# Optimization experiments

Hardware: AMD Instinct MI355X
Metric: run time of the kernel (lower is better)

## Reference

```python
import jax, jax.numpy as jnp
import numpy as np

N_HEADS, D_MODEL, D_HEAD = 16, 1024, 64
BATCH, SEQ = 8, 1024
INIT_RANGE = 0.02
IGNORE = -100000.0


def setup_inputs() -> dict:
    key = jax.random.key(0)
    ks = jax.random.split(key, 6)
    return {
        "normalized_resid_pre": jax.random.normal(ks[0], (BATCH, SEQ, D_MODEL), jnp.float32),
        "encoder_output": jax.random.normal(ks[1], (BATCH, SEQ, D_MODEL), jnp.float32),
        "Qs": jax.random.normal(ks[2], (N_HEADS, D_MODEL, D_HEAD), jnp.float32) * INIT_RANGE,
        "Qbs": jnp.zeros((N_HEADS, D_HEAD), jnp.float32),
        "Ks": jax.random.normal(ks[3], (N_HEADS, D_MODEL, D_HEAD), jnp.float32) * INIT_RANGE,
        "Kbs": jnp.zeros((N_HEADS, D_HEAD), jnp.float32),
        "Vs": jax.random.normal(ks[4], (N_HEADS, D_MODEL, D_HEAD), jnp.float32) * INIT_RANGE,
        "Vbs": jnp.zeros((N_HEADS, D_HEAD), jnp.float32),
        "O": jax.random.normal(ks[5], (N_HEADS, D_HEAD, D_MODEL), jnp.float32) * INIT_RANGE,
        "Ob": jnp.zeros((D_MODEL,), jnp.float32),
    }


def reference(normalized_resid_pre, encoder_output, Qs, Qbs, Ks, Kbs, Vs, Vbs, O, Ob):
    sqrt_d_head = np.sqrt(D_HEAD).astype(np.float32)
    # per-head projections: q,k from encoder_output, v from normalized_resid_pre
    q = jnp.einsum('bpd,hdk->bphk', encoder_output, Qs) + Qbs
    k = jnp.einsum('bpd,hdk->bphk', encoder_output, Ks) + Kbs
    v = jnp.einsum('bpd,hdk->bphk', normalized_resid_pre, Vs) + Vbs
    # [B,H,Q,K] scores, scaled then causally masked with -1e5 (not -inf)
    scores = jnp.einsum('bqhk,bmhk->bhqm', q, k) / sqrt_d_head
    causal = jnp.triu(jnp.ones((SEQ, SEQ), bool), k=1)
    scores = jnp.where(causal, jnp.float32(IGNORE), scores)
    attn = jax.nn.softmax(scores, axis=-1)
    z = jnp.einsum('bmhk,bhqm->bqhk', v, attn)
    return jnp.einsum('bqhk,hkd->bqd', z, O) + Ob
```

## Files before the change

kernel.cpp:

```cpp
#include <hip/hip_runtime.h>
#include <hip/hip_bf16.h>
#include <cstdint>
#include <cstddef>
#include <math.h>


typedef __attribute__((ext_vector_type(8))) short short8;
typedef __attribute__((ext_vector_type(4))) short short4v;
typedef __attribute__((ext_vector_type(4))) float f32x4;

#define MFMA16(A, B, C) __builtin_amdgcn_mfma_f32_16x16x32_bf16(A, B, C, 0, 0, 0)

__device__ inline short f2bs(float f) {
    __bf16 h = (__bf16)f;
    return __builtin_bit_cast(short, h);
}

typedef const __attribute__((address_space(1))) unsigned int* as1_u32p;
typedef __attribute__((address_space(3))) unsigned int* as3_u32p;

__device__ inline void gload_lds16(const void* g, void* lds_base) {
    __builtin_amdgcn_global_load_lds((as1_u32p)(uintptr_t)g,
                                     (as3_u32p)(uintptr_t)lds_base, 16, 0, 0);
}

#define ATTN_SC 0.18033688f
#define ATTN_THR 11.5415603f

__global__ __launch_bounds__(256) void cvt_k(const float* __restrict__ a,
                                             const float* __restrict__ b,
                                             short* __restrict__ oa,
                                             short* __restrict__ ob) {
    const int n = 8 * 1024 * 1024;
    const float* src = blockIdx.y ? b : a;
    short* dst = blockIdx.y ? ob : oa;
    for (int i = (blockIdx.x * 256 + threadIdx.x) * 8; i < n; i += gridDim.x * 256 * 8) {
        f32x4 v0 = *(const f32x4*)(src + i), v1 = *(const f32x4*)(src + i + 4);
        short8 o;
        o[0] = f2bs(v0[0]); o[1] = f2bs(v0[1]); o[2] = f2bs(v0[2]); o[3] = f2bs(v0[3]);
        o[4] = f2bs(v1[0]); o[5] = f2bs(v1[1]); o[6] = f2bs(v1[2]); o[7] = f2bs(v1[3]);
        *(short8*)(dst + i) = o;
    }
}

__global__ __launch_bounds__(256) void wtrans_k(
    const float* __restrict__ Wq, const float* __restrict__ Wk,
    const float* __restrict__ Wv, const float* __restrict__ Wo,
    short* __restrict__ TQ, short* __restrict__ TK,
    short* __restrict__ TV, short* __restrict__ TO) {
    __shared__ short tile[64][72];
    const int wsel = blockIdx.y;
    const float* in = wsel == 0 ? Wq : wsel == 1 ? Wk : wsel == 2 ? Wv : Wo;
    short* out = wsel == 0 ? TQ : wsel == 1 ? TK : wsel == 2 ? TV : TO;
    const int h = blockIdx.x >> 4, tk = blockIdx.x & 15;
    const int t = threadIdx.x;
    size_t ioff; int istr, orow0, ocol0;
    if (wsel < 3) { ioff = (size_t)h * 65536 + (size_t)tk * 64 * 64; istr = 64;   orow0 = h * 64;  ocol0 = tk * 64; }
    else          { ioff = (size_t)h * 65536 + (size_t)tk * 64;      istr = 1024; orow0 = tk * 64; ocol0 = h * 64; }
    {
        const int r = t >> 2, c0 = (t & 3) * 16;
        const float* src = in + ioff + (size_t)r * istr + c0;
#pragma unroll
        for (int j = 0; j < 4; j++) {
            f32x4 v = *(const f32x4*)(src + j * 4);
            tile[r][c0 + j * 4 + 0] = f2bs(v[0]);
            tile[r][c0 + j * 4 + 1] = f2bs(v[1]);
            tile[r][c0 + j * 4 + 2] = f2bs(v[2]);
            tile[r][c0 + j * 4 + 3] = f2bs(v[3]);
        }
    }
    __syncthreads();
    {
        const int cc = t >> 2, rb = (t & 3) * 16;
        short8 o0, o1;
#pragma unroll
        for (int j = 0; j < 8; j++) { o0[j] = tile[rb + j][cc]; o1[j] = tile[rb + 8 + j][cc]; }
        short* dst = out + (size_t)(orow0 + cc) * 1024 + ocol0 + rb;
        *(short8*)dst = o0;
        *(short8*)(dst + 8) = o1;
    }
}

template <int MODE>
__global__ __launch_bounds__(256) void gemm_bt(const short* __restrict__ A,
                                               const short* __restrict__ B,
                                               const float* __restrict__ bias,
                                               void* __restrict__ Cp,
                                               const float* __restrict__ bias2,
                                               void* __restrict__ Cp2) {
    constexpr int K = 1024;
    __shared__ short As[128 * 64];
    __shared__ short Bs[128 * 64];
    const int t = threadIdx.x, l = t & 63, w = t >> 6, lr = l & 15, lg = l >> 4;
    const int wm = (w >> 1) * 64, wn = (w & 1) * 64;
    const int m0 = blockIdx.x * 128, n0 = blockIdx.y * 128;
    const int sr = l >> 3, cb = l & 7;
    f32x4 acc[4][4] = {};

    for (int k0 = 0; k0 < K; k0 += 64) {
#pragma unroll
        for (int i = 0; i < 4; i++) {
            const int c = w * 4 + i, r = c * 8 + sr, cbs = cb ^ (r & 7);
            gload_lds16(A + (size_t)(m0 + r) * K + k0 + cbs * 8, &As[c * 512]);
        }
#pragma unroll
        for (int i = 0; i < 4; i++) {
            const int c = w * 4 + i, r = c * 8 + sr, cbs = cb ^ (r & 7);
            gload_lds16(B + (size_t)(n0 + r) * K + k0 + cbs * 8, &Bs[c * 512]);
        }
        __syncthreads();
#pragma unroll
        for (int kk = 0; kk < 2; kk++) {
            short8 af[4], bf[4];
#pragma unroll
            for (int mi = 0; mi < 4; mi++) {
                const int r = wm + mi * 16 + lr;
                af[mi] = *(const short8*)&As[r * 64 + ((kk * 4 + lg) ^ (r & 7)) * 8];
            }
#pragma unroll
            for (int nj = 0; nj < 4; nj++) {
                const int r = wn + nj * 16 + lr;
                bf[nj] = *(const short8*)&Bs[r * 64 + ((kk * 4 + lg) ^ (r & 7)) * 8];
            }
#pragma unroll
            for (int mi = 0; mi < 4; mi++)
#pragma unroll
                for (int nj = 0; nj < 4; nj++)
                    acc[mi][nj] = MFMA16(af[mi], bf[nj], acc[mi][nj]);
        }
        __syncthreads();
    }

#pragma unroll
    for (int mi = 0; mi < 4; mi++) {
#pragma unroll
        for (int nj = 0; nj < 4; nj++) {
            const int col = n0 + wn + nj * 16 + lr;
            if (MODE == 3) {
                const int h2 = col >> 6;
                short* dst = (short*)(h2 < 16 ? Cp : Cp2);
                const float bv = h2 < 16 ? bias[col & 1023] : bias2[col & 1023];
                const float sc = h2 < 16 ? ATTN_SC : 1.0f;
                const int h = h2 & 15, d = col & 63;
#pragma unroll
                for (int e = 0; e < 4; e++) {
                    const int row = m0 + wm + mi * 16 + lg * 4 + e;
                    const int bb = row >> 10, s = row & 1023;
                    dst[((size_t)(bb * 16 + h) * 1024 + s) * 64 + d] =
                        f2bs((acc[mi][nj][e] + bv) * sc);
                }
            } else if (MODE == 2) {
                const float bv = bias[col];
                const int rowb = m0 + wm + mi * 16 + lg * 4;
                const int bb = rowb >> 10, s0 = rowb & 1023;
                const int h = col >> 6, d = col & 63;
                short4v pk;
#pragma unroll
                for (int e = 0; e < 4; e++) pk[e] = f2bs(acc[mi][nj][e] + bv);
                *(short4v*)((short*)Cp + ((size_t)(bb * 16 + h) * 64 + d) * 1024 + s0) = pk;
            } else {
                const float bv = bias[col];
#pragma unroll
                for (int e = 0; e < 4; e++) {
                    const int row = m0 + wm + mi * 16 + lg * 4 + e;
                    ((float*)Cp)[(size_t)row * 1024 + col] = acc[mi][nj][e] + bv;
                }
            }
        }
    }
}

template <bool DIAG>
__device__ __forceinline__ void attn_tile(
    const short* __restrict__ Ks, const short* __restrict__ Vt,
    short (*__restrict__ Psw)[76],
    const short8* __restrict__ qf, float* __restrict__ m,
    float* __restrict__ ps, f32x4* __restrict__ acc,
    int lr, int lg, int rowloc) {
    f32x4 sf[4];
#pragma unroll
    for (int n = 0; n < 4; n++) {
        const int rk = n * 16 + lr;
        short8 kf0 = *(const short8*)&Ks[rk * 64 + ((lg) ^ (rk & 7)) * 8];
        short8 kf1 = *(const short8*)&Ks[rk * 64 + ((4 + lg) ^ (rk & 7)) * 8];
        f32x4 s = {};
        s = MFMA16(qf[0], kf0, s);
        s = MFMA16(qf[1], kf1, s);
        sf[n] = s;
    }
    if (DIAG) {
#pragma unroll
        for (int n = 0; n < 4; n++)
#pragma unroll
            for (int e = 0; e < 4; e++)
                if (n * 16 + lr > rowloc + e) sf[n][e] = -1e30f;
    }
    float pm[4];
#pragma unroll
    for (int e = 0; e < 4; e++)
        pm[e] = fmaxf(fmaxf(sf[0][e], sf[1][e]), fmaxf(sf[2][e], sf[3][e]));
    bool ok = true;
#pragma unroll
    for (int e = 0; e < 4; e++) ok = ok && (pm[e] <= m[e] + ATTN_THR);
    if (!__all(ok)) {
#pragma unroll
        for (int e = 0; e < 4; e++) {
            float tm = pm[e];
#pragma unroll
            for (int off = 1; off < 16; off <<= 1)
                tm = fmaxf(tm, __shfl_xor(tm, off));
            float nm = fmaxf(m[e], tm);
            float al = exp2f(m[e] - nm);
            m[e] = nm;
            ps[e] *= al;
#pragma unroll
            for (int n4 = 0; n4 < 4; n4++) acc[n4][e] *= al;
        }
    }
#pragma unroll
    for (int e = 0; e < 4; e++) {
#pragma unroll
        for (int n = 0; n < 4; n++) {
            float p = exp2f(sf[n][e] - m[e]);
            ps[e] += p;
            Psw[lg * 4 + e][n * 16 + lr] = f2bs(p);
        }
    }
#pragma unroll
    for (int c = 0; c < 2; c++) {
        short8 pf = *(const short8*)&Psw[lr][lg * 8 + c * 32];
#pragma unroll
        for (int n4 = 0; n4 < 4; n4++) {
            const int rv = n4 * 16 + lr;
            short8 vf = *(const short8*)&Vt[rv * 64 + ((lg + 4 * c) ^ (rv & 7)) * 8];
            acc[n4] = MFMA16(pf, vf, acc[n4]);
        }
    }
}

__global__ __launch_bounds__(256, 4) void attn_k(const short* __restrict__ Q,
                                                 const short* __restrict__ Kp,
                                                 const short* __restrict__ Vg,
                                                 short* __restrict__ Z) {
    __shared__ short Ks[64 * 64];
    __shared__ short Vt[64 * 64];
    __shared__ short Ps[4][16][76];
    const int t = threadIdx.x, l = t & 63, w = t >> 6, lr = l & 15, lg = l >> 4;
    const int bh = blockIdx.x;
    const int qb = 15 - blockIdx.y;
    const int q0 = qb * 64;
    const size_t base = (size_t)bh * 65536;
    const int sr = l >> 3, cb = l & 7;
    const int rowloc = w * 16 + lg * 4;

    short8 qf[2];
    {
        const short* qp = Q + base + (size_t)(q0 + w * 16 + lr) * 64 + lg * 8;
        qf[0] = *(const short8*)qp;
        qf[1] = *(const short8*)(qp + 32);
    }

    float m[4], ps[4];
    f32x4 acc[4] = {};
#pragma unroll
    for (int e = 0; e < 4; e++) { m[e] = -1e30f; ps[e] = 0.f; }

    for (int kt = 0; kt <= qb; kt++) {
        const int k0 = kt * 64;
#pragma unroll
        for (int i = 0; i < 2; i++) {
            const int c = w * 2 + i, r = c * 8 + sr, cbs = cb ^ (r & 7);
            gload_lds16(Kp + base + (size_t)(k0 + r) * 64 + cbs * 8, &Ks[c * 512]);
            gload_lds16(Vg + base + (size_t)r * 1024 + k0 + cbs * 8, &Vt[c * 512]);
        }
        __syncthreads();
        if (kt == qb)
            attn_tile<true>(Ks, Vt, Ps[w], qf, m, ps, acc, lr, lg, rowloc);
        else
            attn_tile<false>(Ks, Vt, Ps[w], qf, m, ps, acc, lr, lg, rowloc);
        __syncthreads();
    }

    const int b = bh >> 4, h = bh & 15;
#pragma unroll
    for (int e = 0; e < 4; e++) {
        float s = ps[e];
#pragma unroll
        for (int off = 1; off < 16; off <<= 1) s += __shfl_xor(s, off);
        ps[e] = 1.f / s;
    }
#pragma unroll
    for (int n4 = 0; n4 < 4; n4++)
#pragma unroll
        for (int e = 0; e < 4; e++) {
            const int rloc = w * 16 + lg * 4 + e;
            Z[((size_t)(b * 1024 + q0 + rloc)) * 1024 + h * 64 + n4 * 16 + lr] =
                f2bs(acc[n4][e] * ps[e]);
        }
}

extern "C" void kernel_launch(void* const* d_in, const int* in_sizes, int n_in,
                              void* d_out, int out_size, void* d_ws, size_t ws_size,
                              hipStream_t stream) {
    const float* resid = (const float*)d_in[0];
    const float* enc   = (const float*)d_in[1];
    const float* Qs    = (const float*)d_in[2];
    const float* Qbs   = (const float*)d_in[3];
    const float* Ksw   = (const float*)d_in[4];
    const float* Kbs   = (const float*)d_in[5];
    const float* Vs    = (const float*)d_in[6];
    const float* Vbs   = (const float*)d_in[7];
    const float* Ow    = (const float*)d_in[8];
    const float* Ob    = (const float*)d_in[9];
    float* out = (float*)d_out;

    char* ws = (char*)d_ws;
    const size_t M16 = (size_t)16 * 1024 * 1024;
    short* Aenc = (short*)ws;
    short* Ares = (short*)(ws + M16);
    short* Qw   = (short*)(ws + 2 * M16);
    short* Kw   = (short*)(ws + 3 * M16);
    short* Vw   = (short*)(ws + 4 * M16);
    short* WqT  = (short*)(ws + 5 * M16);
    short* WkT  = (short*)(ws + 5 * M16 + 2 * 1024 * 1024);
    short* WvT  = (short*)(ws + 5 * M16 + 4 * 1024 * 1024);
    short* WoT  = (short*)(ws + 5 * M16 + 6 * 1024 * 1024);
    short* Zw   = Aenc;

    cvt_k<<<dim3(2048, 2), 256, 0, stream>>>(enc, resid, Aenc, Ares);
    wtrans_k<<<dim3(256, 4), 256, 0, stream>>>(Qs, Ksw, Vs, Ow, WqT, WkT, WvT, WoT);
    gemm_bt<3><<<dim3(64, 16), 256, 0, stream>>>(Aenc, WqT, Qbs, Qw, Kbs, Kw);
    gemm_bt<2><<<dim3(64, 8), 256, 0, stream>>>(Ares, WvT, Vbs, Vw, nullptr, nullptr);
    attn_k<<<dim3(128, 16), 256, 0, stream>>>(Qw, Kw, Vw, Zw);
    gemm_bt<0><<<dim3(64, 8), 256, 0, stream>>>(Zw, WoT, Ob, out, nullptr, nullptr);
}
```

Before: 170.8 us.

## Process two 16-row query strips per wave in attention with 2-wave blocks

The attention kernel now uses 128-thread blocks where each wave handles 32 query rows as two 16-row strips, so each K and V fragment read from LDS feeds two MFMAs. This halves LDS fragment reads per MFMA and cuts the number of waves sharing each K/V tile load. In exchange it roughly doubles accumulator and softmax state registers per lane, lowers the occupancy hint, and gives each block fewer waves to hide load latency, since each thread now issues twice as many global-to-LDS copies.

```diff
diff --git a/kernel.cpp b/kernel.cpp
--- a/kernel.cpp
+++ b/kernel.cpp
@@ -171,132 +171,148 @@
 }
 
 template <bool DIAG>
-__device__ __forceinline__ void attn_tile(
+__device__ __forceinline__ void attn_tile2(
     const short* __restrict__ Ks, const short* __restrict__ Vt,
     short (*__restrict__ Psw)[76],
-    const short8* __restrict__ qf, float* __restrict__ m,
-    float* __restrict__ ps, f32x4* __restrict__ acc,
-    int lr, int lg, int rowloc) {
-    f32x4 sf[4];
+    const short8 (*__restrict__ qf)[2], float (*__restrict__ m)[4],
+    float (*__restrict__ ps)[4], f32x4 (*__restrict__ acc)[4],
+    int lr, int lg, int rowbase) {
+    f32x4 sf[2][4];
 #pragma unroll
     for (int n = 0; n < 4; n++) {
         const int rk = n * 16 + lr;
         short8 kf0 = *(const short8*)&Ks[rk * 64 + ((lg) ^ (rk & 7)) * 8];
         short8 kf1 = *(const short8*)&Ks[rk * 64 + ((4 + lg) ^ (rk & 7)) * 8];
-        f32x4 s = {};
-        s = MFMA16(qf[0], kf0, s);
-        s = MFMA16(qf[1], kf1, s);
-        sf[n] = s;
-    }
-    if (DIAG) {
-#pragma unroll
-        for (int n = 0; n < 4; n++)
-#pragma unroll
-            for (int e = 0; e < 4; e++)
-                if (n * 16 + lr > rowloc + e) sf[n][e] = -1e30f;
-    }
-    float pm[4];
-#pragma unroll
-    for (int e = 0; e < 4; e++)
-        pm[e] = fmaxf(fmaxf(sf[0][e], sf[1][e]), fmaxf(sf[2][e], sf[3][e]));
-    bool ok = true;
-#pragma unroll
-    for (int e = 0; e < 4; e++) ok = ok && (pm[e] <= m[e] + ATTN_THR);
-    if (!__all(ok)) {
+#pragma unroll
+        for (int s = 0; s < 2; s++) {
+            f32x4 a = {};
+            a = MFMA16(qf[s][0], kf0, a);
+            a = MFMA16(qf[s][1], kf1, a);
+            sf[s][n] = a;
+        }
+    }
+#pragma unroll
+    for (int s = 0; s < 2; s++) {
+        const int rowloc = rowbase + s * 16 + lg * 4;
+        if (DIAG) {
+#pragma unroll
+            for (int n = 0; n < 4; n++)
+#pragma unroll
+                for (int e = 0; e < 4; e++)
+                    if (n * 16 + lr > rowloc + e) sf[s][n][e] = -1e30f;
+        }
+        float pm[4];
+#pragma unroll
+        for (int e = 0; e < 4; e++)
+            pm[e] = fmaxf(fmaxf(sf[s][0][e], sf[s][1][e]),
+                          fmaxf(sf[s][2][e], sf[s][3][e]));
+        bool ok = true;
+#pragma unroll
+        for (int e = 0; e < 4; e++) ok = ok && (pm[e] <= m[s][e] + ATTN_THR);
+        if (!__all(ok)) {
+#pragma unroll
+            for (int e = 0; e < 4; e++) {
+                float tm = pm[e];
+#pragma unroll
+                for (int off = 1; off < 16; off <<= 1)
+                    tm = fmaxf(tm, __shfl_xor(tm, off));
+                float nm = fmaxf(m[s][e], tm);
+                float al = exp2f(m[s][e] - nm);
+                m[s][e] = nm;
+                ps[s][e] *= al;
+#pragma unroll
+                for (int n4 = 0; n4 < 4; n4++) acc[s][n4][e] *= al;
+            }
+        }
 #pragma unroll
         for (int e = 0; e < 4; e++) {
-            float tm = pm[e];
-#pragma unroll
-            for (int off = 1; off < 16; off <<= 1)
-                tm = fmaxf(tm, __shfl_xor(tm, off));
-            float nm = fmaxf(m[e], tm);
-            float al = exp2f(m[e] - nm);
-            m[e] = nm;
-            ps[e] *= al;
-#pragma unroll
-            for (int n4 = 0; n4 < 4; n4++) acc[n4][e] *= al;
-        }
-    }
-#pragma unroll
-    for (int e = 0; e < 4; e++) {
-#pragma unroll
-        for (int n = 0; n < 4; n++) {
-            float p = exp2f(sf[n][e] - m[e]);
-            ps[e] += p;
-            Psw[lg * 4 + e][n * 16 + lr] = f2bs(p);
+#pragma unroll
+            for (int n = 0; n < 4; n++) {
+                float p = exp2f(sf[s][n][e] - m[s][e]);
+                ps[s][e] += p;
+                Psw[s * 16 + lg * 4 + e][n * 16 + lr] = f2bs(p);
+            }
         }
     }
 #pragma unroll
     for (int c = 0; c < 2; c++) {
-        short8 pf = *(const short8*)&Psw[lr][lg * 8 + c * 32];
+        short8 pf0 = *(const short8*)&Psw[lr][lg * 8 + c * 32];
+        short8 pf1 = *(const short8*)&Psw[16 + lr][lg * 8 + c * 32];
 #pragma unroll
         for (int n4 = 0; n4 < 4; n4++) {
             const int rv = n4 * 16 + lr;
             short8 vf = *(const short8*)&Vt[rv * 64 + ((lg + 4 * c) ^ (rv & 7)) * 8];
-            acc[n4] = MFMA16(pf, vf, acc[n4]);
-        }
-    }
-}
-
-__global__ __launch_bounds__(256, 4) void attn_k(const short* __restrict__ Q,
+            acc[0][n4] = MFMA16(pf0, vf, acc[0][n4]);
+            acc[1][n4] = MFMA16(pf1, vf, acc[1][n4]);
+        }
+    }
+}
+
+__global__ __launch_bounds__(128, 3) void attn_k(const short* __restrict__ Q,
                                                  const short* __restrict__ Kp,
                                                  const short* __restrict__ Vg,
                                                  short* __restrict__ Z) {
     __shared__ short Ks[64 * 64];
     __shared__ short Vt[64 * 64];
-    __shared__ short Ps[4][16][76];
+    __shared__ short Ps[2][32][76];
     const int t = threadIdx.x, l = t & 63, w = t >> 6, lr = l & 15, lg = l >> 4;
     const int bh = blockIdx.x;
     const int qb = 15 - blockIdx.y;
     const int q0 = qb * 64;
     const size_t base = (size_t)bh * 65536;
     const int sr = l >> 3, cb = l & 7;
-    const int rowloc = w * 16 + lg * 4;
-
-    short8 qf[2];
-    {
-        const short* qp = Q + base + (size_t)(q0 + w * 16 + lr) * 64 + lg * 8;
-        qf[0] = *(const short8*)qp;
-        qf[1] = *(const short8*)(qp + 32);
-    }
-
-    float m[4], ps[4];
-    f32x4 acc[4] = {};
-#pragma unroll
-    for (int e = 0; e < 4; e++) { m[e] = -1e30f; ps[e] = 0.f; }
+    const int rowbase = w * 32;
+
+    short8 qf[2][2];
+#pragma unroll
+    for (int s = 0; s < 2; s++) {
+        const short* qp = Q + base + (size_t)(q0 + w * 32 + s * 16 + lr) * 64 + lg * 8;
+        qf[s][0] = *(const short8*)qp;
+        qf[s][1] = *(const short8*)(qp + 32);
+    }
+
+    float m[2][4], ps[2][4];
+    f32x4 acc[2][4] = {};
+#pragma unroll
+    for (int s = 0; s < 2; s++)
+#pragma unroll
+        for (int e = 0; e < 4; e++) { m[s][e] = -1e30f; ps[s][e] = 0.f; }
 
     for (int kt = 0; kt <= qb; kt++) {
         const int k0 = kt * 64;
 #pragma unroll
-        for (int i = 0; i < 2; i++) {
-            const int c = w * 2 + i, r = c * 8 + sr, cbs = cb ^ (r & 7);
+        for (int i = 0; i < 4; i++) {
+            const int c = w * 4 + i, r = c * 8 + sr, cbs = cb ^ (r & 7);
             gload_lds16(Kp + base + (size_t)(k0 + r) * 64 + cbs * 8, &Ks[c * 512]);
             gload_lds16(Vg + base + (size_t)r * 1024 + k0 + cbs * 8, &Vt[c * 512]);
         }
         __syncthreads();
         if (kt == qb)
-            attn_tile<true>(Ks, Vt, Ps[w], qf, m, ps, acc, lr, lg, rowloc);
+            attn_tile2<true>(Ks, Vt, Ps[w], qf, m, ps, acc, lr, lg, rowbase);
         else
-            attn_tile<false>(Ks, Vt, Ps[w], qf, m, ps, acc, lr, lg, rowloc);
+            attn_tile2<false>(Ks, Vt, Ps[w], qf, m, ps, acc, lr, lg, rowbase);
         __syncthreads();
     }
 
     const int b = bh >> 4, h = bh & 15;
 #pragma unroll
-    for (int e = 0; e < 4; e++) {
-        float s = ps[e];
-#pragma unroll
-        for (int off = 1; off < 16; off <<= 1) s += __shfl_xor(s, off);
-        ps[e] = 1.f / s;
-    }
-#pragma unroll
-    for (int n4 = 0; n4 < 4; n4++)
+    for (int s = 0; s < 2; s++) {
 #pragma unroll
         for (int e = 0; e < 4; e++) {
-            const int rloc = w * 16 + lg * 4 + e;
-            Z[((size_t)(b * 1024 + q0 + rloc)) * 1024 + h * 64 + n4 * 16 + lr] =
-                f2bs(acc[n4][e] * ps[e]);
-        }
+            float sv = ps[s][e];
+#pragma unroll
+            for (int off = 1; off < 16; off <<= 1) sv += __shfl_xor(sv, off);
+            ps[s][e] = 1.f / sv;
+        }
+#pragma unroll
+        for (int n4 = 0; n4 < 4; n4++)
+#pragma unroll
+            for (int e = 0; e < 4; e++) {
+                const int row = q0 + w * 32 + s * 16 + lg * 4 + e;
+                Z[((size_t)(b * 1024 + row)) * 1024 + h * 64 + n4 * 16 + lr] =
+                    f2bs(acc[s][n4][e] * ps[s][e]);
+            }
+    }
 }
 
 extern "C" void kernel_launch(void* const* d_in, const int* in_sizes, int n_in,
@@ -331,6 +347,6 @@
     wtrans_k<<<dim3(256, 4), 256, 0, stream>>>(Qs, Ksw, Vs, Ow, WqT, WkT, WvT, WoT);
     gemm_bt<3><<<dim3(64, 16), 256, 0, stream>>>(Aenc, WqT, Qbs, Qw, Kbs, Kw);
     gemm_bt<2><<<dim3(64, 8), 256, 0, stream>>>(Ares, WvT, Vbs, Vw, nullptr, nullptr);
-    attn_k<<<dim3(128, 16), 256, 0, stream>>>(Qw, Kw, Vw, Zw);
+    attn_k<<<dim3(128, 16), 128, 0, stream>>>(Qw, Kw, Vw, Zw);
     gemm_bt<0><<<dim3(64, 8), 256, 0, stream>>>(Zw, WoT, Ob, out, nullptr, nullptr);
 }
```

New measurement: 181.3 us. 1.06x slower.

## Read K and V fragments directly from global memory in attention loop

Applied to the files above, without the earlier changes.

The attention kernel no longer stages K and V tiles into shared memory with async global-to-LDS loads and block barriers. Each wave now loads its MFMA operand fragments straight from global memory, relying on the L1/L2 caches, and the two __syncthreads per tile are removed. The P scratch row padding shrinks from 76 to 72. The cost is that each of the four waves re-reads the same K/V tile from global/cache, and there is no explicit prefetch, so load latency is more exposed.

```diff
diff --git a/kernel.cpp b/kernel.cpp
--- a/kernel.cpp
+++ b/kernel.cpp
@@ -172,8 +172,9 @@
 
 template <bool DIAG>
 __device__ __forceinline__ void attn_tile(
-    const short* __restrict__ Ks, const short* __restrict__ Vt,
-    short (*__restrict__ Psw)[76],
+    const short* __restrict__ Kt,
+    const short* __restrict__ Vt,
+    short (*__restrict__ Psw)[72],
     const short8* __restrict__ qf, float* __restrict__ m,
     float* __restrict__ ps, f32x4* __restrict__ acc,
     int lr, int lg, int rowloc) {
@@ -181,8 +182,8 @@
 #pragma unroll
     for (int n = 0; n < 4; n++) {
         const int rk = n * 16 + lr;
-        short8 kf0 = *(const short8*)&Ks[rk * 64 + ((lg) ^ (rk & 7)) * 8];
-        short8 kf1 = *(const short8*)&Ks[rk * 64 + ((4 + lg) ^ (rk & 7)) * 8];
+        short8 kf0 = *(const short8*)(Kt + rk * 64 + lg * 8);
+        short8 kf1 = *(const short8*)(Kt + rk * 64 + 32 + lg * 8);
         f32x4 s = {};
         s = MFMA16(qf[0], kf0, s);
         s = MFMA16(qf[1], kf1, s);
@@ -232,7 +233,7 @@
 #pragma unroll
         for (int n4 = 0; n4 < 4; n4++) {
             const int rv = n4 * 16 + lr;
-            short8 vf = *(const short8*)&Vt[rv * 64 + ((lg + 4 * c) ^ (rv & 7)) * 8];
+            short8 vf = *(const short8*)(Vt + (size_t)rv * 1024 + c * 32 + lg * 8);
             acc[n4] = MFMA16(pf, vf, acc[n4]);
         }
     }
@@ -242,15 +243,12 @@
                                                  const short* __restrict__ Kp,
                                                  const short* __restrict__ Vg,
                                                  short* __restrict__ Z) {
-    __shared__ short Ks[64 * 64];
-    __shared__ short Vt[64 * 64];
-    __shared__ short Ps[4][16][76];
+    __shared__ short Ps[4][16][72];
     const int t = threadIdx.x, l = t & 63, w = t >> 6, lr = l & 15, lg = l >> 4;
     const int bh = blockIdx.x;
     const int qb = 15 - blockIdx.y;
     const int q0 = qb * 64;
     const size_t base = (size_t)bh * 65536;
-    const int sr = l >> 3, cb = l & 7;
     const int rowloc = w * 16 + lg * 4;
 
     short8 qf[2];
@@ -265,21 +263,12 @@
 #pragma unroll
     for (int e = 0; e < 4; e++) { m[e] = -1e30f; ps[e] = 0.f; }
 
-    for (int kt = 0; kt <= qb; kt++) {
-        const int k0 = kt * 64;
-#pragma unroll
-        for (int i = 0; i < 2; i++) {
-            const int c = w * 2 + i, r = c * 8 + sr, cbs = cb ^ (r & 7);
-            gload_lds16(Kp + base + (size_t)(k0 + r) * 64 + cbs * 8, &Ks[c * 512]);
-            gload_lds16(Vg + base + (size_t)r * 1024 + k0 + cbs * 8, &Vt[c * 512]);
-        }
-        __syncthreads();
-        if (kt == qb)
-            attn_tile<true>(Ks, Vt, Ps[w], qf, m, ps, acc, lr, lg, rowloc);
-        else
-            attn_tile<false>(Ks, Vt, Ps[w], qf, m, ps, acc, lr, lg, rowloc);
-        __syncthreads();
-    }
+    for (int kt = 0; kt < qb; kt++) {
+        attn_tile<false>(Kp + base + (size_t)kt * 64 * 64, Vg + base + kt * 64,
+                         Ps[w], qf, m, ps, acc, lr, lg, rowloc);
+    }
+    attn_tile<true>(Kp + base + (size_t)qb * 64 * 64, Vg + base + qb * 64,
+                    Ps[w], qf, m, ps, acc, lr, lg, rowloc);
 
     const int b = bh >> 4, h = bh & 15;
 #pragma unroll
```

After: 245.3 us. 1.44x slower.
